# Performance work log

Hardware: AMD Instinct MI355X
Metric: run time of the kernel (lower is better)

The kernel has to match this reference:

```python
import jax, jax.numpy as jnp
import numpy as np

B, N, F, D, M, R, K, TOPR = 32, 1024, 10, 64, 4, 8, 20, 2
TAU = 1.0
BN_EPS = 1e-5


def setup_inputs() -> dict:
    key = jax.random.key(0)
    ks = jax.random.split(key, 20)
    s = 0.1
    p = {}
    p['data'] = jax.random.normal(ks[0], (B, N, F), jnp.float32)
    u = jnp.clip(jax.random.uniform(ks[1], (B, M), jnp.float32), 1e-6, 1.0 - 1e-6)
    p['gumbel_noise'] = -jnp.log(-jnp.log(u))
    p['W_cond'] = jax.random.normal(ks[2], (F, D), jnp.float32) * s
    p['b_cond'] = jnp.zeros((D,), jnp.float32)
    p['W_ap'] = jax.random.normal(ks[3], (D, D), jnp.float32) * s
    p['b_ap'] = jnp.zeros((D,), jnp.float32)
    p['W_av'] = jax.random.normal(ks[4], (D, 1), jnp.float32) * s
    p['W_r'] = jax.random.normal(ks[5], (D, M), jnp.float32) * s
    p['b_r'] = jnp.zeros((M,), jnp.float32)
    p['e_base'] = jax.random.normal(ks[6], (N, D), jnp.float32) * s
    p['lr_u'] = jax.random.normal(ks[7], (M, N, R), jnp.float32) * s
    p['lr_v'] = jax.random.normal(ks[8], (M, R, D), jnp.float32) * s
    p['W_gnn'] = jax.random.normal(ks[9], (F, D), jnp.float32) * s
    p['att_i'] = jax.random.normal(ks[10], (D,), jnp.float32) * s
    p['att_j'] = jax.random.normal(ks[11], (D,), jnp.float32) * s
    p['att_em_i'] = jax.random.normal(ks[12], (D,), jnp.float32) * s
    p['att_em_j'] = jax.random.normal(ks[13], (D,), jnp.float32) * s
    p['b_gnn'] = jnp.zeros((D,), jnp.float32)
    p['bn1_gamma'] = jnp.ones((D,), jnp.float32)
    p['bn1_beta'] = jnp.zeros((D,), jnp.float32)
    p['node_embed_table'] = jax.random.normal(ks[14], (N, D), jnp.float32) * s
    p['bn_out_gamma'] = jnp.ones((D,), jnp.float32)
    p['bn_out_beta'] = jnp.zeros((D,), jnp.float32)
    p['W_out'] = jax.random.normal(ks[15], (D, 1), jnp.float32) * s
    p['b_out'] = jnp.zeros((1,), jnp.float32)
    return p


def _nan(x):
    return jnp.nan_to_num(x, nan=0.0, posinf=1e4, neginf=-1e4)


def _bn(x, gamma, beta, axes):
    # BatchNorm1d in training mode: biased batch stats over `axes`.
    mu = x.mean(axes, keepdims=True)
    var = x.var(axes, keepdims=True)
    return (x - mu) * jax.lax.rsqrt(var + BN_EPS) * gamma + beta


def reference(data, gumbel_noise, W_cond, b_cond, W_ap, b_ap, W_av, W_r, b_r,
              e_base, lr_u, lr_v, W_gnn, att_i, att_j, att_em_i, att_em_j,
              b_gnn, bn1_gamma, bn1_beta, node_embed_table,
              bn_out_gamma, bn_out_beta, W_out, b_out):
    x_det = jax.lax.stop_gradient(data)                      # data.clone().detach()
    # --- condition attention pooling ---
    h_it = data @ W_cond + b_cond                            # [B,N,D]
    ah = jax.nn.leaky_relu(h_it @ W_ap + b_ap, 0.2)
    e_it = _nan((ah @ W_av)[..., 0])                         # [B,N]
    beta = jax.nn.softmax(e_it, axis=1)
    h_sys = jnp.sum(beta[..., None] * h_it, axis=1)          # [B,D]
    # --- gumbel top-k routing with straight-through ---
    pi_soft = jax.nn.softmax((h_sys @ W_r + b_r + gumbel_noise) / TAU, axis=-1)
    topv, topi = jax.lax.top_k(pi_soft, TOPR)
    pi_hard = jnp.sum(jax.nn.one_hot(topi, M, dtype=pi_soft.dtype) * topv[..., None], axis=1)
    pi_hard = pi_hard / jnp.maximum(pi_hard.sum(-1, keepdims=True), 1e-12)
    pi_t = jax.lax.stop_gradient(pi_hard - pi_soft) + pi_soft
    # --- low-rank expert prototypes -> mixed node embeddings ---
    proto = e_base[None] + jnp.einsum('mnr,mrd->mnd', lr_u, lr_v)    # [M,N,D]
    mixed = _nan(jnp.einsum('bm,mnd->bnd', pi_t, proto))             # [B,N,D]
    # --- dynamic top-k graph construction ---
    scores = _nan(jnp.einsum('bid,bjd->bij', mixed, mixed))          # [B,N,N]
    topk_vals, topk_idx = jax.lax.top_k(scores, K)                   # src nodes per dst: [B,N,K]
    topk_w = jax.nn.softmax(topk_vals, axis=-1)                      # edge weights
    # --- GAT-style layer with embedding-augmented keys, self loops re-added ---
    x_lin = x_det @ W_gnn                                            # [B,N,D]
    s_i = x_lin @ att_i + mixed @ att_em_i                           # [B,N]
    s_j = x_lin @ att_j + mixed @ att_em_j
    sj_nb = jnp.take_along_axis(s_j, topk_idx.reshape(B, N * K), axis=1).reshape(B, N, K)
    self_mask = topk_idx == jnp.arange(N)[None, :, None]             # remove_self_loops on topk edges
    alpha_nb = jnp.where(self_mask, -jnp.inf, jax.nn.leaky_relu(s_i[:, :, None] + sj_nb, 0.2))
    alpha_self = jax.nn.leaky_relu(s_i + s_j, 0.2)
    att = jax.nn.softmax(jnp.concatenate([alpha_nb, alpha_self[..., None]], axis=-1), axis=-1)
    w_nb = att[..., :K] * topk_w                                     # edge_weight modulation
    w_self = att[..., K]
    x_src = jnp.take_along_axis(x_lin, topk_idx.reshape(B, N * K)[..., None], axis=1).reshape(B, N, K, D)
    gnn = jnp.einsum('bnk,bnkd->bnd', w_nb, x_src) + w_self[..., None] * x_lin + b_gnn
    gnn = jax.nn.relu(_bn(gnn.reshape(B * N, D), bn1_gamma, bn1_beta, 0).reshape(B, N, D))
    # --- output head ---
    out = gnn * node_embed_table[None]                               # [B,N,D]
    out = jax.nn.relu(_bn(out, bn_out_gamma, bn_out_beta, (0, 1)))   # dropout = identity (eval)
    out = (out @ W_out + b_out).reshape(-1, N)                       # [B,N]
    return out, h_sys, pi_soft
```

## Files before the change

### kernel.cpp

```cpp
#include <hip/hip_runtime.h>
#include <math.h>

#define BB 32
#define NN 1024
#define FF 10
#define DD 64
#define MM 4
#define RR 8
#define KK 20
#define BNROWS (BB*NN)

#define OFF_HIT   0ull
#define OFF_XLIN  2097152ull
#define OFF_EIT   4194304ull
#define OFF_PIT   4227072ull
#define OFF_MIXED 4227200ull
#define OFF_SI    6324352ull
#define OFF_SJ    6357120ull
#define OFF_GNN   7700608ull
#define OFF_OUTP  9797760ull
#define OFF_STAT  11894912ull
#define OFF_SC    (OFF_STAT + 2560ull)

__device__ __forceinline__ float wave_sum(float v) {
    #pragma unroll
    for (int off = 32; off; off >>= 1) v += __shfl_xor(v, off);
    return v;
}
__device__ __forceinline__ float wave_max(float v) {
    #pragma unroll
    for (int off = 32; off; off >>= 1) v = fmaxf(v, __shfl_xor(v, off));
    return v;
}

__global__ __launch_bounds__(256) void k_rows(
    const float* __restrict__ data, const float* __restrict__ W_cond,
    const float* __restrict__ b_cond, const float* __restrict__ W_ap,
    const float* __restrict__ b_ap, const float* __restrict__ W_av,
    const float* __restrict__ W_gnn,
    float* __restrict__ h_it, float* __restrict__ x_lin, float* __restrict__ e_it,
    float* __restrict__ stats)
{
    if (blockIdx.x < 10) {
        int idx = blockIdx.x * 256 + threadIdx.x;
        if (idx < 2336) stats[idx] = 0.f;
    }
    int w = threadIdx.x >> 6, lane = threadIdx.x & 63;
    int r = blockIdx.x * 4 + w;
    const float* dr = data + r * FF;
    float df[FF];
    #pragma unroll
    for (int f = 0; f < FF; f++) df[f] = dr[f];
    float h = b_cond[lane], x = 0.f;
    #pragma unroll
    for (int f = 0; f < FF; f++) {
        h = fmaf(df[f], W_cond[f * DD + lane], h);
        x = fmaf(df[f], W_gnn[f * DD + lane], x);
    }
    h_it[r * DD + lane] = h;
    x_lin[r * DD + lane] = x;
    float acc = b_ap[lane];
    #pragma unroll
    for (int e2 = 0; e2 < DD; e2++)
        acc = fmaf(__shfl(h, e2), W_ap[e2 * DD + lane], acc);
    float lr = acc > 0.f ? acc : 0.2f * acc;
    float ep = wave_sum(lr * W_av[lane]);
    if (lane == 0) e_it[r] = ep;
}

__global__ __launch_bounds__(256) void k_pool2(
    const float* __restrict__ e_it, const float* __restrict__ h_it,
    float* __restrict__ num, float* __restrict__ den)
{
    int w = threadIdx.x >> 6, lane = threadIdx.x & 63;
    int b = blockIdx.x >> 3, ch = blockIdx.x & 7;
    int base = b * NN + ch * 128 + w * 32;
    float acc = 0.f, dn = 0.f;
    #pragma unroll 4
    for (int i = 0; i < 32; i++) {
        float e = e_it[base + i];
        float wgt = expf(e);
        acc = fmaf(wgt, h_it[(size_t)(base + i) * DD + lane], acc);
        dn += wgt;
    }
    __shared__ float pa[4][DD];
    __shared__ float pd[4];
    pa[w][lane] = acc;
    if (lane == 0) pd[w] = dn;
    __syncthreads();
    if (w == 0) {
        float s = pa[0][lane] + pa[1][lane] + pa[2][lane] + pa[3][lane];
        atomicAdd(&num[b * DD + lane], s);
        if (lane == 0) atomicAdd(&den[b], pd[0] + pd[1] + pd[2] + pd[3]);
    }
}

__global__ void k_route(const float* __restrict__ num, const float* __restrict__ den,
                        const float* __restrict__ W_r, const float* __restrict__ b_r,
                        const float* __restrict__ gumbel,
                        float* __restrict__ h_sys, float* __restrict__ pi_soft,
                        float* __restrict__ pi_t)
{
    int tid = threadIdx.x;
    for (int i = tid; i < BB * DD; i += 256)
        h_sys[i] = num[i] / den[i >> 6];
    if (tid >= BB) return;
    int b = tid;
    float inv = 1.0f / den[b];
    float lg[MM];
    #pragma unroll
    for (int m = 0; m < MM; m++) lg[m] = b_r[m] + gumbel[b * MM + m];
    for (int d = 0; d < DD; d++) {
        float hv = num[b * DD + d] * inv;
        #pragma unroll
        for (int m = 0; m < MM; m++) lg[m] = fmaf(hv, W_r[d * MM + m], lg[m]);
    }
    float mx = fmaxf(fmaxf(lg[0], lg[1]), fmaxf(lg[2], lg[3]));
    float s = 0.f, p[MM];
    #pragma unroll
    for (int m = 0; m < MM; m++) { p[m] = expf(lg[m] - mx); s += p[m]; }
    #pragma unroll
    for (int m = 0; m < MM; m++) { p[m] /= s; pi_soft[b * MM + m] = p[m]; }
    int i1 = 0; float v1 = p[0];
    #pragma unroll
    for (int m = 1; m < MM; m++) if (p[m] > v1) { v1 = p[m]; i1 = m; }
    int i2 = -1; float v2 = -1.f;
    #pragma unroll
    for (int m = 0; m < MM; m++) if (m != i1 && p[m] > v2) { v2 = p[m]; i2 = m; }
    float norm = fmaxf(v1 + v2, 1e-12f);
    #pragma unroll
    for (int m = 0; m < MM; m++)
        pi_t[b * MM + m] = (m == i1 ? v1 : (m == i2 ? v2 : 0.f)) / norm;
}

__global__ __launch_bounds__(256) void k_mixed(
    const float* __restrict__ e_base, const float* __restrict__ lr_u,
    const float* __restrict__ lr_v, const float* __restrict__ pi_t,
    const float* __restrict__ x_lin,
    const float* __restrict__ att_i, const float* __restrict__ att_j,
    const float* __restrict__ att_em_i, const float* __restrict__ att_em_j,
    float* __restrict__ mixed, float* __restrict__ s_i, float* __restrict__ s_j)
{
    int w = threadIdx.x >> 6, lane = threadIdx.x & 63;
    int r = blockIdx.x * 4 + w;
    int b = r >> 10, n = r & 1023;
    float LR[MM];
    #pragma unroll
    for (int m = 0; m < MM; m++) {
        float a = 0.f;
        #pragma unroll
        for (int rr = 0; rr < RR; rr++)
            a = fmaf(lr_u[(m * NN + n) * RR + rr], lr_v[(m * RR + rr) * DD + lane], a);
        LR[m] = a;
    }
    float eb = e_base[n * DD + lane];
    float mx = 0.f;
    #pragma unroll
    for (int m = 0; m < MM; m++) mx = fmaf(pi_t[b * MM + m], eb + LR[m], mx);
    mixed[(size_t)r * DD + lane] = mx;
    float x = x_lin[(size_t)r * DD + lane];
    float r1 = wave_sum(x * att_i[lane] + mx * att_em_i[lane]);
    float r2 = wave_sum(x * att_j[lane] + mx * att_em_j[lane]);
    if (lane == 0) { s_i[r] = r1; s_j[r] = r2; }
}

__global__ __launch_bounds__(256) void k_score(
    const float* __restrict__ mixed_chunk, float* __restrict__ sc)
{
    __shared__ float As[32 * 132];
    __shared__ float Bs[32 * 132];
    int t = threadIdx.x;
    int bb = blockIdx.x >> 6;
    int rr = blockIdx.x & 63;
    int it = rr >> 3, jt = rr & 7;
    int i0 = it * 128, j0 = jt * 128;
    const float* mb = mixed_chunk + (size_t)bb * NN * DD;

    int tx = t & 15, ty = t >> 4;
    float acc[8][8];
    #pragma unroll
    for (int a = 0; a < 8; a++)
        #pragma unroll
        for (int bj = 0; bj < 8; bj++) acc[a][bj] = 0.f;

    int rowi[4], qi[4], swi[4];
    #pragma unroll
    for (int c = 0; c < 4; c++) {
        int id = t + c * 256;
        rowi[c] = (id & 15) | ((id >> 7) << 4);
        qi[c] = (id >> 4) & 7;
        swi[c] = ((rowi[c] & 4) << 4) | ((rowi[c] >> 3) << 2) | (rowi[c] & 3);
    }

    float4 pa[4], pb[4];
    #pragma unroll
    for (int c = 0; c < 4; c++) {
        pa[c] = *(const float4*)(mb + (size_t)(i0 + rowi[c]) * DD + qi[c] * 4);
        pb[c] = *(const float4*)(mb + (size_t)(j0 + rowi[c]) * DD + qi[c] * 4);
    }
    for (int hh = 0; hh < 2; hh++) {
        if (hh) __syncthreads();
        #pragma unroll
        for (int c = 0; c < 4; c++) {
            int pos = qi[c] * 4 * 132 + swi[c];
            As[pos] = pa[c].x; As[pos + 132] = pa[c].y; As[pos + 264] = pa[c].z; As[pos + 396] = pa[c].w;
            Bs[pos] = pb[c].x; Bs[pos + 132] = pb[c].y; Bs[pos + 264] = pb[c].z; Bs[pos + 396] = pb[c].w;
        }
        __syncthreads();
        if (hh == 0) {
            #pragma unroll
            for (int c = 0; c < 4; c++) {
                pa[c] = *(const float4*)(mb + (size_t)(i0 + rowi[c]) * DD + 32 + qi[c] * 4);
                pb[c] = *(const float4*)(mb + (size_t)(j0 + rowi[c]) * DD + 32 + qi[c] * 4);
            }
        }
        #pragma unroll 4
        for (int d = 0; d < 32; d++) {
            float4 a0 = *(const float4*)&As[d * 132 + ty * 4];
            float4 a1 = *(const float4*)&As[d * 132 + 64 + ty * 4];
            float4 b0 = *(const float4*)&Bs[d * 132 + tx * 4];
            float4 b1 = *(const float4*)&Bs[d * 132 + 64 + tx * 4];
            float av[8] = {a0.x, a0.y, a0.z, a0.w, a1.x, a1.y, a1.z, a1.w};
            float bv[8] = {b0.x, b0.y, b0.z, b0.w, b1.x, b1.y, b1.z, b1.w};
            #pragma unroll
            for (int a = 0; a < 8; a++)
                #pragma unroll
                for (int bj = 0; bj < 8; bj++)
                    acc[a][bj] = fmaf(av[a], bv[bj], acc[a][bj]);
        }
    }

    float* out = sc + ((size_t)bb * NN + i0 + ty * 8) * NN + j0 + tx * 8;
    #pragma unroll
    for (int a = 0; a < 8; a++) {
        float4 o0 = {acc[a][0], acc[a][1], acc[a][2], acc[a][3]};
        float4 o1 = {acc[a][4], acc[a][5], acc[a][6], acc[a][7]};
        *(float4*)(out + (size_t)a * NN) = o0;
        *(float4*)(out + (size_t)a * NN + 4) = o1;
    }
}

__global__ __launch_bounds__(256) void k_selgat(
    const float* __restrict__ sc, int b0,
    const float* __restrict__ x_lin, const float* __restrict__ s_i,
    const float* __restrict__ s_j, const float* __restrict__ b_gnn,
    float* __restrict__ gnn_pre)
{
    int w = threadIdx.x >> 6, lane = threadIdx.x & 63;
    int lr = blockIdx.x * 4 + w;
    int r = b0 * NN + lr;
    int b = r >> 10, n = r & 1023;
    const float* row = sc + (size_t)lr * NN;

    unsigned uk[16];
    #pragma unroll
    for (int c = 0; c < 4; c++) {
        float4 v = *(const float4*)(row + c * 256 + lane * 4);
        float vv[4] = {v.x, v.y, v.z, v.w};
        #pragma unroll
        for (int q = 0; q < 4; q++) {
            unsigned u = __float_as_uint(vv[q]);
            uk[c * 4 + q] = u ^ (((unsigned)((int)u >> 31)) | 0x80000000u);
        }
    }
    unsigned mx = uk[0];
    #pragma unroll
    for (int i = 1; i < 16; i++) mx = uk[i] > mx ? uk[i] : mx;
    unsigned sv = mx;
    #pragma unroll
    for (int blk = 2; blk <= 64; blk <<= 1) {
        #pragma unroll
        for (int dist = blk >> 1; dist >= 1; dist >>= 1) {
            unsigned pv = (unsigned)__shfl_xor((int)sv, dist);
            bool up = (lane & blk) == 0;
            bool upper = (lane & dist) == 0;
            bool g = sv > pv;
            sv = (((g == upper) == up)) ? sv : pv;
        }
    }
    unsigned tau = (unsigned)__shfl((int)sv, 19);

    __shared__ unsigned skey[4][64];
    __shared__ int sjj[4][64];
    int base = 0;
    #pragma unroll
    for (int s = 0; s < 16; s++) {
        bool q = uk[s] >= tau;
        unsigned long long m = __ballot(q);
        if (q) {
            int pos = base + __popcll(m & ((1ull << lane) - 1ull));
            if (pos < 64) {
                skey[w][pos] = uk[s];
                sjj[w][pos] = ((s >> 2) << 8) + lane * 4 + (s & 3);
            }
        }
        base += __popcll(m);
    }
    int C = base;

    float vk = -INFINITY; int ik = 0;
    if (C <= 64) {
        unsigned ck = 0u; int cj = 0x7FFFFFFF;
        if (lane < C) { ck = skey[w][lane]; cj = sjj[w][lane]; }
        if (C <= 32) {
            #pragma unroll
            for (int blk = 2; blk <= 32; blk <<= 1)
                #pragma unroll
                for (int dist = blk >> 1; dist >= 1; dist >>= 1) {
                    unsigned pk = (unsigned)__shfl_xor((int)ck, dist);
                    int pj = __shfl_xor(cj, dist);
                    bool up = (lane & blk) == 0;
                    bool upper = (lane & dist) == 0;
                    bool g = (ck > pk) || (ck == pk && cj < pj);
                    bool keep = ((g == upper) == up);
                    ck = keep ? ck : pk; cj = keep ? cj : pj;
                }
        } else {
            #pragma unroll
            for (int blk = 2; blk <= 64; blk <<= 1)
                #pragma unroll
                for (int dist = blk >> 1; dist >= 1; dist >>= 1) {
                    unsigned pk = (unsigned)__shfl_xor((int)ck, dist);
                    int pj = __shfl_xor(cj, dist);
                    bool up = (lane & blk) == 0;
                    bool upper = (lane & dist) == 0;
                    bool g = (ck > pk) || (ck == pk && cj < pj);
                    bool keep = ((g == upper) == up);
                    ck = keep ? ck : pk; cj = keep ? cj : pj;
                }
        }
        if (lane < KK) {
            unsigned u = (ck & 0x80000000u) ? (ck ^ 0x80000000u) : ~ck;
            vk = __uint_as_float(u);
            ik = cj;
        }
    } else {
        for (int k = 0; k < KK; k++) {
            unsigned bm = uk[0]; int bsl = 0;
            #pragma unroll
            for (int i = 1; i < 16; i++) if (uk[i] > bm) { bm = uk[i]; bsl = i; }
            unsigned wm = bm;
            #pragma unroll
            for (int off = 32; off; off >>= 1) {
                unsigned tt = (unsigned)__shfl_xor((int)wm, off);
                wm = tt > wm ? tt : wm;
            }
            unsigned long long ball = __ballot(bm == wm);
            int winner = (int)__builtin_ctzll(ball);
            int slotw = __shfl(bsl, winner);
            int jw = ((slotw >> 2) << 8) + winner * 4 + (slotw & 3);
            unsigned u2 = (wm & 0x80000000u) ? (wm ^ 0x80000000u) : ~wm;
            if (lane == k) { vk = __uint_as_float(u2); ik = jw; }
            if (lane == winner) uk[bsl] = 0u;
        }
    }

    float m1 = wave_max(vk);
    float ek = (lane < KK) ? expf(vk - m1) : 0.f;
    float s1v = wave_sum(ek);
    float wk = ek / s1v;
    float si = s_i[r], sjn = s_j[r];
    float a = -INFINITY;
    if (lane < KK) {
        float sjk = s_j[(b << 10) + ik];
        float t2 = si + sjk;
        a = (ik == n) ? -INFINITY : (t2 > 0.f ? t2 : 0.2f * t2);
    }
    float ts = si + sjn;
    float aself = ts > 0.f ? ts : 0.2f * ts;
    float am = wave_max(fmaxf(a, aself));
    float ea = (lane < KK && a != -INFINITY) ? expf(a - am) : 0.f;
    float es = expf(aself - am);
    float ssum = wave_sum(ea) + es;
    float wnb = (ea / ssum) * wk;
    float wself = es / ssum;
    float acc = b_gnn[lane] + wself * x_lin[(size_t)r * DD + lane];
    #pragma unroll
    for (int k = 0; k < KK; k++) {
        int jk = __shfl(ik, k);
        float wv = __shfl(wnb, k);
        acc = fmaf(wv, x_lin[((size_t)(b << 10) + jk) * DD + lane], acc);
    }
    gnn_pre[(size_t)r * DD + lane] = acc;
}

__global__ __launch_bounds__(256) void k_stats(const float* __restrict__ src, float* __restrict__ sums)
{
    int w = threadIdx.x >> 6, lane = threadIdx.x & 63;
    __shared__ float ps[4][DD], pq[4][DD];
    float s = 0.f, q = 0.f;
    int base = blockIdx.x * 128;
    for (int i = w; i < 128; i += 4) {
        float v = src[(size_t)(base + i) * DD + lane];
        s += v; q = fmaf(v, v, q);
    }
    ps[w][lane] = s; pq[w][lane] = q;
    __syncthreads();
    if (w == 0) {
        s = ps[0][lane] + ps[1][lane] + ps[2][lane] + ps[3][lane];
        q = pq[0][lane] + pq[1][lane] + pq[2][lane] + pq[3][lane];
        atomicAdd(&sums[lane], s);
        atomicAdd(&sums[DD + lane], q);
    }
}

__global__ __launch_bounds__(256) void k_bn1(
    const float* __restrict__ gnn_pre, float* __restrict__ stats,
    const float* __restrict__ gamma, const float* __restrict__ beta,
    const float* __restrict__ net, float* __restrict__ out_pre)
{
    int tid = threadIdx.x;
    int d0 = (tid & 15) * 4;
    float mean4[4], rs4[4], bt4[4];
    #pragma unroll
    for (int k = 0; k < 4; k++) {
        float mu = stats[d0 + k] * (1.0f / BNROWS);
        float var = stats[64 + d0 + k] * (1.0f / BNROWS) - mu * mu;
        mean4[k] = mu;
        rs4[k] = rsqrtf(var + 1e-5f) * gamma[d0 + k];
        bt4[k] = beta[d0 + k];
    }
    float s4[4] = {0, 0, 0, 0}, q4[4] = {0, 0, 0, 0};
    size_t base4 = (size_t)blockIdx.x * 2048;
    #pragma unroll
    for (int i = 0; i < 8; i++) {
        size_t f4 = base4 + (size_t)i * 256 + tid;
        float4 v = ((const float4*)gnn_pre)[f4];
        int n = ((int)(f4 >> 4)) & 1023;
        float4 nv = ((const float4*)net)[(size_t)n * 16 + (tid & 15)];
        float vv[4] = {v.x, v.y, v.z, v.w};
        float nn2[4] = {nv.x, nv.y, nv.z, nv.w};
        float ov[4];
        #pragma unroll
        for (int k = 0; k < 4; k++) {
            float y = (vv[k] - mean4[k]) * rs4[k] + bt4[k];
            y = y > 0.f ? y : 0.f;
            float o = y * nn2[k];
            ov[k] = o;
            s4[k] += o;
            q4[k] = fmaf(o, o, q4[k]);
        }
        float4 o4 = {ov[0], ov[1], ov[2], ov[3]};
        ((float4*)out_pre)[f4] = o4;
    }
    __shared__ float4 ls[256], lq[256];
    ls[tid] = make_float4(s4[0], s4[1], s4[2], s4[3]);
    lq[tid] = make_float4(q4[0], q4[1], q4[2], q4[3]);
    __syncthreads();
    if (tid < 16) {
        float4 S = ls[tid], Q = lq[tid];
        #pragma unroll
        for (int rr = 1; rr < 16; rr++) {
            float4 a = ls[tid + 16 * rr], b = lq[tid + 16 * rr];
            S.x += a.x; S.y += a.y; S.z += a.z; S.w += a.w;
            Q.x += b.x; Q.y += b.y; Q.z += b.z; Q.w += b.w;
        }
        atomicAdd(&stats[128 + tid * 4 + 0], S.x);
        atomicAdd(&stats[128 + tid * 4 + 1], S.y);
        atomicAdd(&stats[128 + tid * 4 + 2], S.z);
        atomicAdd(&stats[128 + tid * 4 + 3], S.w);
        atomicAdd(&stats[192 + tid * 4 + 0], Q.x);
        atomicAdd(&stats[192 + tid * 4 + 1], Q.y);
        atomicAdd(&stats[192 + tid * 4 + 2], Q.z);
        atomicAdd(&stats[192 + tid * 4 + 3], Q.w);
    }
}

__global__ __launch_bounds__(256) void k_head(
    const float* __restrict__ out_pre, const float* __restrict__ stats,
    const float* __restrict__ gamma, const float* __restrict__ beta,
    const float* __restrict__ W_out, const float* __restrict__ b_out,
    float* __restrict__ out)
{
    int w = threadIdx.x >> 6, lane = threadIdx.x & 63;
    int r = blockIdx.x * 4 + w;
    float mean = stats[lane] * (1.0f / BNROWS);
    float var = stats[DD + lane] * (1.0f / BNROWS) - mean * mean;
    float rs = rsqrtf(var + 1e-5f);
    float y = (out_pre[(size_t)r * DD + lane] - mean) * rs * gamma[lane] + beta[lane];
    y = y > 0.f ? y : 0.f;
    float p = wave_sum(y * W_out[lane]);
    if (lane == 0) out[r] = p + b_out[0];
}

extern "C" void kernel_launch(void* const* d_in, const int* in_sizes, int n_in,
                              void* d_out, int out_size, void* d_ws, size_t ws_size,
                              hipStream_t stream)
{
    const float* data     = (const float*)d_in[0];
    const float* gumbel   = (const float*)d_in[1];
    const float* W_cond   = (const float*)d_in[2];
    const float* b_cond   = (const float*)d_in[3];
    const float* W_ap     = (const float*)d_in[4];
    const float* b_ap     = (const float*)d_in[5];
    const float* W_av     = (const float*)d_in[6];
    const float* W_r      = (const float*)d_in[7];
    const float* b_r      = (const float*)d_in[8];
    const float* e_base   = (const float*)d_in[9];
    const float* lr_u     = (const float*)d_in[10];
    const float* lr_v     = (const float*)d_in[11];
    const float* W_gnn    = (const float*)d_in[12];
    const float* att_i    = (const float*)d_in[13];
    const float* att_j    = (const float*)d_in[14];
    const float* att_em_i = (const float*)d_in[15];
    const float* att_em_j = (const float*)d_in[16];
    const float* b_gnn    = (const float*)d_in[17];
    const float* bn1_g    = (const float*)d_in[18];
    const float* bn1_b    = (const float*)d_in[19];
    const float* net      = (const float*)d_in[20];
    const float* bno_g    = (const float*)d_in[21];
    const float* bno_b    = (const float*)d_in[22];
    const float* W_out    = (const float*)d_in[23];
    const float* b_out    = (const float*)d_in[24];

    float* ws = (float*)d_ws;
    float* h_it   = ws + OFF_HIT;
    float* x_lin  = ws + OFF_XLIN;
    float* e_it   = ws + OFF_EIT;
    float* pi_t   = ws + OFF_PIT;
    float* mixed  = ws + OFF_MIXED;
    float* s_i    = ws + OFF_SI;
    float* s_j    = ws + OFF_SJ;
    float* gnn_pre = ws + OFF_GNN;
    float* out_pre = ws + OFF_OUTP;
    float* stats   = ws + OFF_STAT;
    float* pnum    = stats + 256;
    float* pden    = stats + 2304;

    float* out0    = (float*)d_out;
    float* h_sys   = out0 + BB * NN;
    float* pi_soft = out0 + BB * NN + BB * DD;

    k_rows<<<BNROWS / 4, 256, 0, stream>>>(data, W_cond, b_cond, W_ap, b_ap, W_av, W_gnn,
                                           h_it, x_lin, e_it, stats);
    k_pool2<<<BB * 8, 256, 0, stream>>>(e_it, h_it, pnum, pden);
    k_route<<<1, 256, 0, stream>>>(pnum, pden, W_r, b_r, gumbel, h_sys, pi_soft, pi_t);
    k_mixed<<<BNROWS / 4, 256, 0, stream>>>(e_base, lr_u, lr_v, pi_t, x_lin,
                                            att_i, att_j, att_em_i, att_em_j, mixed, s_i, s_j);

    size_t ws_floats = ws_size / 4;
    size_t avail = ws_floats > OFF_SC ? ws_floats - OFF_SC : 0;
    int cb = (int)(avail / (size_t)(NN * NN));
    if (cb > BB) cb = BB;
    float* sc = ws + OFF_SC;
    if (cb < 1) { cb = 2; sc = h_it; }
    for (int b0 = 0; b0 < BB; b0 += cb) {
        int c = (BB - b0) < cb ? (BB - b0) : cb;
        k_score<<<c * 64, 256, 0, stream>>>(mixed + (size_t)b0 * NN * DD, sc);
        k_selgat<<<c * 256, 256, 0, stream>>>(sc, b0, x_lin, s_i, s_j, b_gnn, gnn_pre);
    }

    k_stats<<<256, 256, 0, stream>>>(gnn_pre, stats);
    k_bn1<<<256, 256, 0, stream>>>(gnn_pre, stats, bn1_g, bn1_b, net, out_pre);
    k_head<<<BNROWS / 4, 256, 0, stream>>>(out_pre, stats + 128, bno_g, bno_b, W_out, b_out, out0);
}
```

Measured before the change: 319.8 us.

## Fuse attention pooling, routing and BN stats into neighboring kernels; halve score K-tile

Folds the attention-pooling reduction into k_rows, which now accumulates exp-weighted h into pnum/pden with atomics instead of writing h_it and e_it. The routing softmax and top-2 selection are recomputed per wave inside k_mixed, removing the k_pool2 and k_route launches. BN1 statistics are accumulated inside k_selgat, replacing k_stats. The stats buffer is now zeroed with a memset, and k_score stages K in 16-wide chunks to cut shared memory, at the cost of more barriers. The trade-off is many more atomics in k_rows and redundant routing math in every k_mixed wave.

```diff
diff --git a/kernel.cpp b/kernel.cpp
--- a/kernel.cpp
+++ b/kernel.cpp
@@ -12,8 +12,6 @@
 
 #define OFF_HIT   0ull
 #define OFF_XLIN  2097152ull
-#define OFF_EIT   4194304ull
-#define OFF_PIT   4227072ull
 #define OFF_MIXED 4227200ull
 #define OFF_SI    6324352ull
 #define OFF_SJ    6357120ull
@@ -38,15 +36,11 @@
     const float* __restrict__ b_cond, const float* __restrict__ W_ap,
     const float* __restrict__ b_ap, const float* __restrict__ W_av,
     const float* __restrict__ W_gnn,
-    float* __restrict__ h_it, float* __restrict__ x_lin, float* __restrict__ e_it,
-    float* __restrict__ stats)
-{
-    if (blockIdx.x < 10) {
-        int idx = blockIdx.x * 256 + threadIdx.x;
-        if (idx < 2336) stats[idx] = 0.f;
-    }
+    float* __restrict__ x_lin, float* __restrict__ pnum, float* __restrict__ pden)
+{
     int w = threadIdx.x >> 6, lane = threadIdx.x & 63;
     int r = blockIdx.x * 4 + w;
+    int b = r >> 10;
     const float* dr = data + r * FF;
     float df[FF];
     #pragma unroll
@@ -57,7 +51,6 @@
         h = fmaf(df[f], W_cond[f * DD + lane], h);
         x = fmaf(df[f], W_gnn[f * DD + lane], x);
     }
-    h_it[r * DD + lane] = h;
     x_lin[r * DD + lane] = x;
     float acc = b_ap[lane];
     #pragma unroll
@@ -65,85 +58,86 @@
         acc = fmaf(__shfl(h, e2), W_ap[e2 * DD + lane], acc);
     float lr = acc > 0.f ? acc : 0.2f * acc;
     float ep = wave_sum(lr * W_av[lane]);
-    if (lane == 0) e_it[r] = ep;
-}
-
-__global__ __launch_bounds__(256) void k_pool2(
-    const float* __restrict__ e_it, const float* __restrict__ h_it,
-    float* __restrict__ num, float* __restrict__ den)
-{
-    int w = threadIdx.x >> 6, lane = threadIdx.x & 63;
-    int b = blockIdx.x >> 3, ch = blockIdx.x & 7;
-    int base = b * NN + ch * 128 + w * 32;
-    float acc = 0.f, dn = 0.f;
-    #pragma unroll 4
-    for (int i = 0; i < 32; i++) {
-        float e = e_it[base + i];
-        float wgt = expf(e);
-        acc = fmaf(wgt, h_it[(size_t)(base + i) * DD + lane], acc);
-        dn += wgt;
-    }
+    float wgt = expf(ep);
+
     __shared__ float pa[4][DD];
     __shared__ float pd[4];
-    pa[w][lane] = acc;
-    if (lane == 0) pd[w] = dn;
+    pa[w][lane] = wgt * h;
+    if (lane == 0) pd[w] = wgt;
     __syncthreads();
     if (w == 0) {
         float s = pa[0][lane] + pa[1][lane] + pa[2][lane] + pa[3][lane];
-        atomicAdd(&num[b * DD + lane], s);
-        if (lane == 0) atomicAdd(&den[b], pd[0] + pd[1] + pd[2] + pd[3]);
-    }
-}
-
-__global__ void k_route(const float* __restrict__ num, const float* __restrict__ den,
-                        const float* __restrict__ W_r, const float* __restrict__ b_r,
-                        const float* __restrict__ gumbel,
-                        float* __restrict__ h_sys, float* __restrict__ pi_soft,
-                        float* __restrict__ pi_t)
-{
-    int tid = threadIdx.x;
-    for (int i = tid; i < BB * DD; i += 256)
-        h_sys[i] = num[i] / den[i >> 6];
-    if (tid >= BB) return;
-    int b = tid;
-    float inv = 1.0f / den[b];
-    float lg[MM];
-    #pragma unroll
-    for (int m = 0; m < MM; m++) lg[m] = b_r[m] + gumbel[b * MM + m];
-    for (int d = 0; d < DD; d++) {
-        float hv = num[b * DD + d] * inv;
-        #pragma unroll
-        for (int m = 0; m < MM; m++) lg[m] = fmaf(hv, W_r[d * MM + m], lg[m]);
-    }
-    float mx = fmaxf(fmaxf(lg[0], lg[1]), fmaxf(lg[2], lg[3]));
-    float s = 0.f, p[MM];
-    #pragma unroll
-    for (int m = 0; m < MM; m++) { p[m] = expf(lg[m] - mx); s += p[m]; }
-    #pragma unroll
-    for (int m = 0; m < MM; m++) { p[m] /= s; pi_soft[b * MM + m] = p[m]; }
-    int i1 = 0; float v1 = p[0];
-    #pragma unroll
-    for (int m = 1; m < MM; m++) if (p[m] > v1) { v1 = p[m]; i1 = m; }
-    int i2 = -1; float v2 = -1.f;
-    #pragma unroll
-    for (int m = 0; m < MM; m++) if (m != i1 && p[m] > v2) { v2 = p[m]; i2 = m; }
-    float norm = fmaxf(v1 + v2, 1e-12f);
-    #pragma unroll
-    for (int m = 0; m < MM; m++)
-        pi_t[b * MM + m] = (m == i1 ? v1 : (m == i2 ? v2 : 0.f)) / norm;
+        atomicAdd(&pnum[b * DD + lane], s);
+        if (lane == 0) atomicAdd(&pden[b], pd[0] + pd[1] + pd[2] + pd[3]);
+    }
 }
 
 __global__ __launch_bounds__(256) void k_mixed(
     const float* __restrict__ e_base, const float* __restrict__ lr_u,
-    const float* __restrict__ lr_v, const float* __restrict__ pi_t,
+    const float* __restrict__ lr_v,
+    const float* __restrict__ pnum, const float* __restrict__ pden,
+    const float* __restrict__ gumbel, const float* __restrict__ W_r,
+    const float* __restrict__ b_r,
     const float* __restrict__ x_lin,
     const float* __restrict__ att_i, const float* __restrict__ att_j,
     const float* __restrict__ att_em_i, const float* __restrict__ att_em_j,
-    float* __restrict__ mixed, float* __restrict__ s_i, float* __restrict__ s_j)
-{
-    int w = threadIdx.x >> 6, lane = threadIdx.x & 63;
+    float* __restrict__ mixed, float* __restrict__ s_i, float* __restrict__ s_j,
+    float* __restrict__ h_sys, float* __restrict__ pi_soft)
+{
+    int t = threadIdx.x, w = t >> 6, lane = t & 63;
     int r = blockIdx.x * 4 + w;
     int b = r >> 10, n = r & 1023;
+
+    float inv = 1.0f / pden[b];
+    float lg[MM];
+    #pragma unroll
+    for (int m = 0; m < MM; m++) lg[m] = b_r[m] + gumbel[b * MM + m];
+    for (int d = 0; d < DD; d++) {
+        float hv = pnum[b * DD + d] * inv;
+        #pragma unroll
+        for (int m = 0; m < MM; m++) lg[m] = fmaf(hv, W_r[d * MM + m], lg[m]);
+    }
+    float mxl = fmaxf(fmaxf(lg[0], lg[1]), fmaxf(lg[2], lg[3]));
+    float sp = 0.f, p[MM];
+    #pragma unroll
+    for (int m = 0; m < MM; m++) { p[m] = expf(lg[m] - mxl); sp += p[m]; }
+    #pragma unroll
+    for (int m = 0; m < MM; m++) p[m] /= sp;
+    int i1 = 0; float v1 = p[0];
+    #pragma unroll
+    for (int m = 1; m < MM; m++) if (p[m] > v1) { v1 = p[m]; i1 = m; }
+    int i2 = -1; float v2 = -1.f;
+    #pragma unroll
+    for (int m = 0; m < MM; m++) if (m != i1 && p[m] > v2) { v2 = p[m]; i2 = m; }
+    float norm = fmaxf(v1 + v2, 1e-12f);
+    float pt[MM];
+    #pragma unroll
+    for (int m = 0; m < MM; m++)
+        pt[m] = (m == i1 ? v1 : (m == i2 ? v2 : 0.f)) / norm;
+
+    if (blockIdx.x == 0) {
+        for (int i = t; i < BB * DD; i += 256)
+            h_sys[i] = pnum[i] / pden[i >> 6];
+        if (t < BB) {
+            int b2 = t;
+            float inv2 = 1.0f / pden[b2];
+            float lg2[MM];
+            #pragma unroll
+            for (int m = 0; m < MM; m++) lg2[m] = b_r[m] + gumbel[b2 * MM + m];
+            for (int d = 0; d < DD; d++) {
+                float hv = pnum[b2 * DD + d] * inv2;
+                #pragma unroll
+                for (int m = 0; m < MM; m++) lg2[m] = fmaf(hv, W_r[d * MM + m], lg2[m]);
+            }
+            float mx2 = fmaxf(fmaxf(lg2[0], lg2[1]), fmaxf(lg2[2], lg2[3]));
+            float s2 = 0.f, p2[MM];
+            #pragma unroll
+            for (int m = 0; m < MM; m++) { p2[m] = expf(lg2[m] - mx2); s2 += p2[m]; }
+            #pragma unroll
+            for (int m = 0; m < MM; m++) pi_soft[b2 * MM + m] = p2[m] / s2;
+        }
+    }
+
     float LR[MM];
     #pragma unroll
     for (int m = 0; m < MM; m++) {
@@ -156,7 +150,7 @@
     float eb = e_base[n * DD + lane];
     float mx = 0.f;
     #pragma unroll
-    for (int m = 0; m < MM; m++) mx = fmaf(pi_t[b * MM + m], eb + LR[m], mx);
+    for (int m = 0; m < MM; m++) mx = fmaf(pt[m], eb + LR[m], mx);
     mixed[(size_t)r * DD + lane] = mx;
     float x = x_lin[(size_t)r * DD + lane];
     float r1 = wave_sum(x * att_i[lane] + mx * att_em_i[lane]);
@@ -167,8 +161,8 @@
 __global__ __launch_bounds__(256) void k_score(
     const float* __restrict__ mixed_chunk, float* __restrict__ sc)
 {
-    __shared__ float As[32 * 132];
-    __shared__ float Bs[32 * 132];
+    __shared__ float As[16 * 132];
+    __shared__ float Bs[16 * 132];
     int t = threadIdx.x;
     int bb = blockIdx.x >> 6;
     int rr = blockIdx.x & 63;
@@ -183,39 +177,39 @@
         #pragma unroll
         for (int bj = 0; bj < 8; bj++) acc[a][bj] = 0.f;
 
-    int rowi[4], qi[4], swi[4];
-    #pragma unroll
-    for (int c = 0; c < 4; c++) {
+    int rowi[2], qi[2], swi[2];
+    #pragma unroll
+    for (int c = 0; c < 2; c++) {
         int id = t + c * 256;
-        rowi[c] = (id & 15) | ((id >> 7) << 4);
-        qi[c] = (id >> 4) & 7;
+        qi[c] = (id >> 4) & 3;
+        rowi[c] = (id & 15) | ((id >> 6) << 4);
         swi[c] = ((rowi[c] & 4) << 4) | ((rowi[c] >> 3) << 2) | (rowi[c] & 3);
     }
-
-    float4 pa[4], pb[4];
-    #pragma unroll
-    for (int c = 0; c < 4; c++) {
+    float4 pa[2], pb[2];
+    #pragma unroll
+    for (int c = 0; c < 2; c++) {
         pa[c] = *(const float4*)(mb + (size_t)(i0 + rowi[c]) * DD + qi[c] * 4);
         pb[c] = *(const float4*)(mb + (size_t)(j0 + rowi[c]) * DD + qi[c] * 4);
     }
-    for (int hh = 0; hh < 2; hh++) {
-        if (hh) __syncthreads();
-        #pragma unroll
-        for (int c = 0; c < 4; c++) {
+    #pragma unroll
+    for (int st = 0; st < 4; st++) {
+        if (st) __syncthreads();
+        #pragma unroll
+        for (int c = 0; c < 2; c++) {
             int pos = qi[c] * 4 * 132 + swi[c];
             As[pos] = pa[c].x; As[pos + 132] = pa[c].y; As[pos + 264] = pa[c].z; As[pos + 396] = pa[c].w;
             Bs[pos] = pb[c].x; Bs[pos + 132] = pb[c].y; Bs[pos + 264] = pb[c].z; Bs[pos + 396] = pb[c].w;
         }
         __syncthreads();
-        if (hh == 0) {
-            #pragma unroll
-            for (int c = 0; c < 4; c++) {
-                pa[c] = *(const float4*)(mb + (size_t)(i0 + rowi[c]) * DD + 32 + qi[c] * 4);
-                pb[c] = *(const float4*)(mb + (size_t)(j0 + rowi[c]) * DD + 32 + qi[c] * 4);
+        if (st < 3) {
+            #pragma unroll
+            for (int c = 0; c < 2; c++) {
+                pa[c] = *(const float4*)(mb + (size_t)(i0 + rowi[c]) * DD + (st + 1) * 16 + qi[c] * 4);
+                pb[c] = *(const float4*)(mb + (size_t)(j0 + rowi[c]) * DD + (st + 1) * 16 + qi[c] * 4);
             }
         }
         #pragma unroll 4
-        for (int d = 0; d < 32; d++) {
+        for (int d = 0; d < 16; d++) {
             float4 a0 = *(const float4*)&As[d * 132 + ty * 4];
             float4 a1 = *(const float4*)&As[d * 132 + 64 + ty * 4];
             float4 b0 = *(const float4*)&Bs[d * 132 + tx * 4];
@@ -244,7 +238,7 @@
     const float* __restrict__ sc, int b0,
     const float* __restrict__ x_lin, const float* __restrict__ s_i,
     const float* __restrict__ s_j, const float* __restrict__ b_gnn,
-    float* __restrict__ gnn_pre)
+    float* __restrict__ gnn_pre, float* __restrict__ stats)
 {
     int w = threadIdx.x >> 6, lane = threadIdx.x & 63;
     int lr = blockIdx.x * 4 + w;
@@ -374,33 +368,24 @@
     float ssum = wave_sum(ea) + es;
     float wnb = (ea / ssum) * wk;
     float wself = es / ssum;
-    float acc = b_gnn[lane] + wself * x_lin[(size_t)r * DD + lane];
+    float accg = b_gnn[lane] + wself * x_lin[(size_t)r * DD + lane];
     #pragma unroll
     for (int k = 0; k < KK; k++) {
         int jk = __shfl(ik, k);
         float wv = __shfl(wnb, k);
-        acc = fmaf(wv, x_lin[((size_t)(b << 10) + jk) * DD + lane], acc);
-    }
-    gnn_pre[(size_t)r * DD + lane] = acc;
-}
-
-__global__ __launch_bounds__(256) void k_stats(const float* __restrict__ src, float* __restrict__ sums)
-{
-    int w = threadIdx.x >> 6, lane = threadIdx.x & 63;
-    __shared__ float ps[4][DD], pq[4][DD];
-    float s = 0.f, q = 0.f;
-    int base = blockIdx.x * 128;
-    for (int i = w; i < 128; i += 4) {
-        float v = src[(size_t)(base + i) * DD + lane];
-        s += v; q = fmaf(v, v, q);
-    }
-    ps[w][lane] = s; pq[w][lane] = q;
+        accg = fmaf(wv, x_lin[((size_t)(b << 10) + jk) * DD + lane], accg);
+    }
+    gnn_pre[(size_t)r * DD + lane] = accg;
+
+    __shared__ float spart[2][4][64];
+    spart[0][w][lane] = accg;
+    spart[1][w][lane] = accg * accg;
     __syncthreads();
     if (w == 0) {
-        s = ps[0][lane] + ps[1][lane] + ps[2][lane] + ps[3][lane];
-        q = pq[0][lane] + pq[1][lane] + pq[2][lane] + pq[3][lane];
-        atomicAdd(&sums[lane], s);
-        atomicAdd(&sums[DD + lane], q);
+        float S = spart[0][0][lane] + spart[0][1][lane] + spart[0][2][lane] + spart[0][3][lane];
+        float Q = spart[1][0][lane] + spart[1][1][lane] + spart[1][2][lane] + spart[1][3][lane];
+        atomicAdd(&stats[lane], S);
+        atomicAdd(&stats[64 + lane], Q);
     }
 }
 
@@ -514,13 +499,10 @@
     const float* b_out    = (const float*)d_in[24];
 
     float* ws = (float*)d_ws;
-    float* h_it   = ws + OFF_HIT;
-    float* x_lin  = ws + OFF_XLIN;
-    float* e_it   = ws + OFF_EIT;
-    float* pi_t   = ws + OFF_PIT;
-    float* mixed  = ws + OFF_MIXED;
-    float* s_i    = ws + OFF_SI;
-    float* s_j    = ws + OFF_SJ;
+    float* x_lin   = ws + OFF_XLIN;
+    float* mixed   = ws + OFF_MIXED;
+    float* s_i     = ws + OFF_SI;
+    float* s_j     = ws + OFF_SJ;
     float* gnn_pre = ws + OFF_GNN;
     float* out_pre = ws + OFF_OUTP;
     float* stats   = ws + OFF_STAT;
@@ -531,26 +513,26 @@
     float* h_sys   = out0 + BB * NN;
     float* pi_soft = out0 + BB * NN + BB * DD;
 
+    hipMemsetAsync(stats, 0, 2336 * sizeof(float), stream);
+
     k_rows<<<BNROWS / 4, 256, 0, stream>>>(data, W_cond, b_cond, W_ap, b_ap, W_av, W_gnn,
-                                           h_it, x_lin, e_it, stats);
-    k_pool2<<<BB * 8, 256, 0, stream>>>(e_it, h_it, pnum, pden);
-    k_route<<<1, 256, 0, stream>>>(pnum, pden, W_r, b_r, gumbel, h_sys, pi_soft, pi_t);
-    k_mixed<<<BNROWS / 4, 256, 0, stream>>>(e_base, lr_u, lr_v, pi_t, x_lin,
-                                            att_i, att_j, att_em_i, att_em_j, mixed, s_i, s_j);
+                                           x_lin, pnum, pden);
+    k_mixed<<<BNROWS / 4, 256, 0, stream>>>(e_base, lr_u, lr_v, pnum, pden, gumbel, W_r, b_r,
+                                            x_lin, att_i, att_j, att_em_i, att_em_j,
+                                            mixed, s_i, s_j, h_sys, pi_soft);
 
     size_t ws_floats = ws_size / 4;
     size_t avail = ws_floats > OFF_SC ? ws_floats - OFF_SC : 0;
     int cb = (int)(avail / (size_t)(NN * NN));
     if (cb > BB) cb = BB;
     float* sc = ws + OFF_SC;
-    if (cb < 1) { cb = 2; sc = h_it; }
+    if (cb < 1) { cb = 2; sc = ws + OFF_HIT; }
     for (int b0 = 0; b0 < BB; b0 += cb) {
         int c = (BB - b0) < cb ? (BB - b0) : cb;
         k_score<<<c * 64, 256, 0, stream>>>(mixed + (size_t)b0 * NN * DD, sc);
-        k_selgat<<<c * 256, 256, 0, stream>>>(sc, b0, x_lin, s_i, s_j, b_gnn, gnn_pre);
-    }
-
-    k_stats<<<256, 256, 0, stream>>>(gnn_pre, stats);
+        k_selgat<<<c * 256, 256, 0, stream>>>(sc, b0, x_lin, s_i, s_j, b_gnn, gnn_pre, stats);
+    }
+
     k_bn1<<<256, 256, 0, stream>>>(gnn_pre, stats, bn1_g, bn1_b, net, out_pre);
     k_head<<<BNROWS / 4, 256, 0, stream>>>(out_pre, stats + 128, bno_g, bno_b, W_out, b_out, out0);
 }
```

Measured after the change: 542.4 us. +69.6%, slower.
